# Performance work log

Measured on AMD Instinct MI355X. Metric: run time of the kernel, lower is better.

## Reference

```python
import jax, jax.numpy as jnp
import numpy as np

C = 1024        # BIGNET_DIM
GS = 128        # group_size
R = 4           # lora_dim
NL = 12         # 4 blocks x 3 QLoRALinear
N = 4096        # batch
NG = C * C // GS  # 8192 groups per layer
EPS = 1e-5


def dequant4(q4, norm):
    # q4: [NG, GS//2] int32 in [0,255] (two nibbles per byte), norm: [NG,1] f32
    low = q4 & 0xF
    high = (q4 >> 4) & 0xF
    # interleave: even positions = low nibble, odd = high nibble
    q8 = jnp.stack([low, high], axis=-1).reshape(q4.shape[0], GS)
    w = (q8.astype(jnp.float32) / 15.0 * 2.0 - 1.0) * norm
    return w.reshape(C, C)  # [out_features, in_features]


def qlora_linear(x, q4, norm, a, b):
    # base 4-bit dequant matmul + low-rank LoRA add (bias=False)
    w = dequant4(q4, norm)
    return x @ w.T + (x @ a.T) @ b.T  # [N,C]


def block(x, q4s, norms, As, Bs):
    h = qlora_linear(x, q4s[0], norms[0], As[0], Bs[0])
    h = jax.nn.relu(h)
    h = qlora_linear(h, q4s[1], norms[1], As[1], Bs[1])
    h = jax.nn.relu(h)
    h = qlora_linear(h, q4s[2], norms[2], As[2], Bs[2])
    return h + x  # residual


def layer_norm(x, g, b):
    mu = jnp.mean(x, axis=-1, keepdims=True)
    var = jnp.var(x, axis=-1, keepdims=True)
    return (x - mu) * jax.lax.rsqrt(var + EPS) * g + b


def setup_inputs() -> dict:
    key = jax.random.key(0)
    ks = jax.random.split(key, 5)
    x = jax.random.normal(ks[0], (N, C), dtype=jnp.float32)
    w_q4 = jax.random.randint(ks[1], (NL, NG, GS // 2), 0, 256, dtype=jnp.int32)
    w_norm = jax.random.uniform(ks[2], (NL, NG, 1), dtype=jnp.float32, minval=0.01, maxval=0.1)
    lora_a = jax.random.normal(ks[3], (NL, R, C), dtype=jnp.float32) * 0.02
    lora_b = jax.random.normal(ks[4], (NL, C, R), dtype=jnp.float32) * 0.02
    ln_g = jnp.ones((2, C), dtype=jnp.float32)
    ln_b = jnp.zeros((2, C), dtype=jnp.float32)
    return {"x": x, "w_q4": w_q4, "w_norm": w_norm, "lora_a": lora_a,
            "lora_b": lora_b, "ln_g": ln_g, "ln_b": ln_b}


def reference(x, w_q4, w_norm, lora_a, lora_b, ln_g, ln_b):
    h = block(x, w_q4[0:3], w_norm[0:3], lora_a[0:3], lora_b[0:3])
    h = layer_norm(h, ln_g[0], ln_b[0])
    h = block(h, w_q4[3:6], w_norm[3:6], lora_a[3:6], lora_b[3:6])
    h = block(h, w_q4[6:9], w_norm[6:9], lora_a[6:9], lora_b[6:9])
    h = layer_norm(h, ln_g[1], ln_b[1])
    h = block(h, w_q4[9:12], w_norm[9:12], lora_a[9:12], lora_b[9:12])
    return h
```

## Files before the change

### kernel.cpp

```cpp
#include <hip/hip_runtime.h>

#define CD 1024
#define NB 4096

typedef __attribute__((ext_vector_type(8))) short short8;
typedef __attribute__((ext_vector_type(4))) short short4v;
typedef __attribute__((ext_vector_type(4))) float f32x4;
typedef __attribute__((ext_vector_type(4))) int int4v;

typedef __attribute__((address_space(1))) const void gv_t;
typedef __attribute__((address_space(3))) void lv_t;
#define GLOAD16(g, l) __builtin_amdgcn_global_load_lds((gv_t*)(g), (lv_t*)(l), 16, 0, 0)

__device__ __forceinline__ short f2bf(float f) {
  unsigned u = __float_as_uint(f);
  u = (u + 0x7FFFu + ((u >> 16) & 1u)) >> 16;
  return (short)u;
}
__device__ __forceinline__ float bf2f(short s) {
  return __uint_as_float(((unsigned)(unsigned short)s) << 16);
}

__global__ __launch_bounds__(256) void prep_kernel(const float* __restrict__ x,
                                                   short* __restrict__ xb,
                                                   const int* __restrict__ q4,
                                                   const float* __restrict__ nrm,
                                                   const float* __restrict__ la,
                                                   const float* __restrict__ lb,
                                                   short* __restrict__ Wb) {
  int bid = blockIdx.x;
  if (bid < 2048) {
    int i = (bid * 256 + threadIdx.x) * 8;
    f32x4 a = *(const f32x4*)(x + i);
    f32x4 b = *(const f32x4*)(x + i + 4);
    short8 o;
    o[0] = f2bf(a[0]); o[1] = f2bf(a[1]); o[2] = f2bf(a[2]); o[3] = f2bf(a[3]);
    o[4] = f2bf(b[0]); o[5] = f2bf(b[1]); o[6] = f2bf(b[2]); o[7] = f2bf(b[3]);
    *(short8*)(xb + i) = o;
    return;
  }
  int tidg = (bid - 2048) * 256 + threadIdx.x;
  int w0 = tidg * 4;
  int l = w0 >> 19;
  int wl = w0 & 524287;
  int g = wl >> 6;
  int j0 = wl & 63;
  int o = g >> 3;
  int kb = ((g & 7) << 7) + (j0 << 1);
  int4v q = *(const int4v*)(q4 + w0);
  float n = nrm[(l << 13) + g];
  float s = n * (2.0f / 15.0f);
  f32x4 B = *(const f32x4*)(lb + (((l << 10) + o) << 2));
  const float* A = la + (l << 12);
  float Ar[4][8];
#pragma unroll
  for (int r = 0; r < 4; ++r) {
    f32x4 u = *(const f32x4*)(A + r * CD + kb);
    f32x4 v = *(const f32x4*)(A + r * CD + kb + 4);
    Ar[r][0] = u[0]; Ar[r][1] = u[1]; Ar[r][2] = u[2]; Ar[r][3] = u[3];
    Ar[r][4] = v[0]; Ar[r][5] = v[1]; Ar[r][6] = v[2]; Ar[r][7] = v[3];
  }
  short8 outv;
#pragma unroll
  for (int p = 0; p < 8; ++p) {
    int qw = q[p >> 1];
    int nib = (qw >> ((p & 1) << 2)) & 15;
    float wv = (float)nib * s - n;
    wv += B[0] * Ar[0][p] + B[1] * Ar[1][p] + B[2] * Ar[2][p] + B[3] * Ar[3][p];
    outv[p] = f2bf(wv);
  }
  *(short8*)(Wb + (l << 20) + (o << 10) + kb) = outv;
}

template <int EPI>
__global__ __launch_bounds__(512) void qgemm(const short* __restrict__ Act,
                                             const short* __restrict__ W,
                                             const short* __restrict__ Res,
                                             void* __restrict__ Out) {
  __shared__ __align__(16) short ldsA[2][2][128 * 64];
  __shared__ __align__(16) short ldsB[2][2][128 * 64];
  const int tid = threadIdx.x;
  const int lane = tid & 63;
  const int wid = tid >> 6;
  const int wr = wid >> 2;
  const int wc = wid & 3;
  const int f = blockIdx.x;
  const int xcd = f & 7, c = f >> 3;
  const int m0 = (((xcd << 2) | (c & 3)) << 7);
  const int o0 = ((c >> 2) << 7);

  const short* aptr[2][2];
  const short* bptr[2][2];
#pragma unroll
  for (int h = 0; h < 2; ++h)
#pragma unroll
    for (int i = 0; i < 2; ++i) {
      int cc = tid + (i << 9);
      int row = cc >> 3;
      int ch = (cc & 7) ^ (row & 7);
      aptr[h][i] = Act + (long)(m0 + row) * CD + (h << 6) + (ch << 3);
      bptr[h][i] = W + (long)(o0 + row) * CD + (h << 6) + (ch << 3);
    }

  auto stage = [&](int t, int buf) {
    const int koff = t << 7;
#pragma unroll
    for (int h = 0; h < 2; ++h)
#pragma unroll
      for (int i = 0; i < 2; ++i) {
        GLOAD16(aptr[h][i] + koff, &ldsA[buf][h][(tid + (i << 9)) << 3]);
        GLOAD16(bptr[h][i] + koff, &ldsB[buf][h][(tid + (i << 9)) << 3]);
      }
  };

  f32x4 acc[4][2] = {};
  const int frow = lane & 15;
  const int fch = lane >> 4;
  const int fsw = lane & 7;

  stage(0, 0);
  for (int t = 0; t < 8; ++t) {
    __syncthreads();
    if (t < 7) stage(t + 1, (t + 1) & 1);
#pragma unroll
    for (int kk = 0; kk < 4; ++kk) {
      const short* La = ldsA[t & 1][kk >> 1];
      const short* Lb = ldsB[t & 1][kk >> 1];
      const int chsw = (((kk & 1) << 2) + fch) ^ fsw;
      short8 af[4], wf[2];
#pragma unroll
      for (int m = 0; m < 4; ++m) {
        int row = (wr << 6) + (m << 4) + frow;
        af[m] = *(const short8*)(La + (row << 6) + (chsw << 3));
      }
#pragma unroll
      for (int n = 0; n < 2; ++n) {
        int row = (wc << 5) + (n << 4) + frow;
        wf[n] = *(const short8*)(Lb + (row << 6) + (chsw << 3));
      }
#pragma unroll
      for (int m = 0; m < 4; ++m)
#pragma unroll
        for (int n = 0; n < 2; ++n)
          acc[m][n] = __builtin_amdgcn_mfma_f32_16x16x32_bf16(wf[n], af[m], acc[m][n], 0, 0, 0);
    }
  }

  const int orow = m0 + (wr << 6) + frow;
  const int ocol = o0 + (wc << 5) + (fch << 2);
#pragma unroll
  for (int m = 0; m < 4; ++m) {
#pragma unroll
    for (int n = 0; n < 2; ++n) {
      long row = orow + (m << 4);
      int col = ocol + (n << 4);
      f32x4 v = acc[m][n];
      if (EPI == 0) {
        short4v ov;
        ov[0] = f2bf(fmaxf(v[0], 0.0f));
        ov[1] = f2bf(fmaxf(v[1], 0.0f));
        ov[2] = f2bf(fmaxf(v[2], 0.0f));
        ov[3] = f2bf(fmaxf(v[3], 0.0f));
        *(short4v*)((short*)Out + row * CD + col) = ov;
      } else if (EPI == 2) {
        short4v rv = *(const short4v*)(Res + row * CD + col);
        short4v ov;
        ov[0] = f2bf(v[0] + bf2f(rv[0]));
        ov[1] = f2bf(v[1] + bf2f(rv[1]));
        ov[2] = f2bf(v[2] + bf2f(rv[2]));
        ov[3] = f2bf(v[3] + bf2f(rv[3]));
        *(short4v*)((short*)Out + row * CD + col) = ov;
      } else {
        short4v rv = *(const short4v*)(Res + row * CD + col);
        f32x4 ov;
        ov[0] = v[0] + bf2f(rv[0]);
        ov[1] = v[1] + bf2f(rv[1]);
        ov[2] = v[2] + bf2f(rv[2]);
        ov[3] = v[3] + bf2f(rv[3]);
        *(f32x4*)((float*)Out + row * CD + col) = ov;
      }
    }
  }
}

__global__ __launch_bounds__(256) void ln_kernel(const short* __restrict__ in,
                                                 short* __restrict__ out,
                                                 const float* __restrict__ g,
                                                 const float* __restrict__ b) {
  __shared__ float rs_[4], rq_[4];
  int row = blockIdx.x, tid = threadIdx.x;
  int k = tid * 4;
  short4v v = *(const short4v*)(in + (long)row * CD + k);
  float f0 = bf2f(v[0]), f1 = bf2f(v[1]), f2 = bf2f(v[2]), f3 = bf2f(v[3]);
  float s = f0 + f1 + f2 + f3;
  float q = f0 * f0 + f1 * f1 + f2 * f2 + f3 * f3;
#pragma unroll
  for (int off = 1; off < 64; off <<= 1) {
    s += __shfl_xor(s, off);
    q += __shfl_xor(q, off);
  }
  if ((tid & 63) == 0) { rs_[tid >> 6] = s; rq_[tid >> 6] = q; }
  __syncthreads();
  s = rs_[0] + rs_[1] + rs_[2] + rs_[3];
  q = rq_[0] + rq_[1] + rq_[2] + rq_[3];
  float mu = s * (1.0f / 1024.0f);
  float var = q * (1.0f / 1024.0f) - mu * mu;
  float rstd = rsqrtf(var + 1e-5f);
  short4v o;
  o[0] = f2bf((f0 - mu) * rstd * g[k] + b[k]);
  o[1] = f2bf((f1 - mu) * rstd * g[k + 1] + b[k + 1]);
  o[2] = f2bf((f2 - mu) * rstd * g[k + 2] + b[k + 2]);
  o[3] = f2bf((f3 - mu) * rstd * g[k + 3] + b[k + 3]);
  *(short4v*)(out + (long)row * CD + k) = o;
}

extern "C" void kernel_launch(void* const* d_in, const int* in_sizes, int n_in,
                              void* d_out, int out_size, void* d_ws, size_t ws_size,
                              hipStream_t stream) {
  const float* x = (const float*)d_in[0];
  const int* q4 = (const int*)d_in[1];
  const float* nrm = (const float*)d_in[2];
  const float* la = (const float*)d_in[3];
  const float* lb = (const float*)d_in[4];
  const float* lng = (const float*)d_in[5];
  const float* lnb = (const float*)d_in[6];

  short* Wb = (short*)d_ws;
  short* buf0 = (short*)((char*)d_ws + (24u << 20));
  short* buf1 = buf0 + (long)NB * CD;
  short* buf2 = (short*)d_out;
  short* buf3 = buf2 + (long)NB * CD;
  float* outf = (float*)d_out;

  prep_kernel<<<dim3(8192), dim3(256), 0, stream>>>(x, buf0, q4, nrm, la, lb, Wb);

  dim3 gg(256), bb(512);
  auto Wl = [&](int l) { return Wb + ((long)l << 20); };

  qgemm<0><<<gg, bb, 0, stream>>>(buf0, Wl(0), nullptr, buf1);
  qgemm<0><<<gg, bb, 0, stream>>>(buf1, Wl(1), nullptr, buf2);
  qgemm<2><<<gg, bb, 0, stream>>>(buf2, Wl(2), buf0, buf3);
  ln_kernel<<<dim3(4096), dim3(256), 0, stream>>>(buf3, buf0, lng, lnb);
  qgemm<0><<<gg, bb, 0, stream>>>(buf0, Wl(3), nullptr, buf1);
  qgemm<0><<<gg, bb, 0, stream>>>(buf1, Wl(4), nullptr, buf2);
  qgemm<2><<<gg, bb, 0, stream>>>(buf2, Wl(5), buf0, buf3);
  qgemm<0><<<gg, bb, 0, stream>>>(buf3, Wl(6), nullptr, buf1);
  qgemm<0><<<gg, bb, 0, stream>>>(buf1, Wl(7), nullptr, buf2);
  qgemm<2><<<gg, bb, 0, stream>>>(buf2, Wl(8), buf3, buf0);
  ln_kernel<<<dim3(4096), dim3(256), 0, stream>>>(buf0, buf1, lng + CD, lnb + CD);
  qgemm<0><<<gg, bb, 0, stream>>>(buf1, Wl(9), nullptr, buf2);
  qgemm<0><<<gg, bb, 0, stream>>>(buf2, Wl(10), nullptr, buf0);
  qgemm<3><<<gg, bb, 0, stream>>>(buf0, Wl(11), buf1, (void*)outf);
}
```

Before: 278.9 us.

## Restructure qgemm main loop into triple-buffered 64-wide K pipeline with manual waitcnts

```diff
diff --git a/kernel.cpp b/kernel.cpp
--- a/kernel.cpp
+++ b/kernel.cpp
@@ -11,6 +11,7 @@
 typedef __attribute__((address_space(1))) const void gv_t;
 typedef __attribute__((address_space(3))) void lv_t;
 #define GLOAD16(g, l) __builtin_amdgcn_global_load_lds((gv_t*)(g), (lv_t*)(l), 16, 0, 0)
+#define MF(a, b, c) __builtin_amdgcn_mfma_f32_16x16x32_bf16((a), (b), (c), 0, 0, 0)
 
 __device__ __forceinline__ short f2bf(float f) {
   unsigned u = __float_as_uint(f);
@@ -77,8 +78,8 @@
                                              const short* __restrict__ W,
                                              const short* __restrict__ Res,
                                              void* __restrict__ Out) {
-  __shared__ __align__(16) short ldsA[2][2][128 * 64];
-  __shared__ __align__(16) short ldsB[2][2][128 * 64];
+  __shared__ __align__(16) short ldsA[3][128 * 64];
+  __shared__ __align__(16) short ldsB[3][128 * 64];
   const int tid = threadIdx.x;
   const int lane = tid & 63;
   const int wid = tid >> 6;
@@ -89,61 +90,87 @@
   const int m0 = (((xcd << 2) | (c & 3)) << 7);
   const int o0 = ((c >> 2) << 7);
 
-  const short* aptr[2][2];
-  const short* bptr[2][2];
-#pragma unroll
-  for (int h = 0; h < 2; ++h)
-#pragma unroll
-    for (int i = 0; i < 2; ++i) {
-      int cc = tid + (i << 9);
-      int row = cc >> 3;
-      int ch = (cc & 7) ^ (row & 7);
-      aptr[h][i] = Act + (long)(m0 + row) * CD + (h << 6) + (ch << 3);
-      bptr[h][i] = W + (long)(o0 + row) * CD + (h << 6) + (ch << 3);
-    }
-
-  auto stage = [&](int t, int buf) {
-    const int koff = t << 7;
-#pragma unroll
-    for (int h = 0; h < 2; ++h)
-#pragma unroll
-      for (int i = 0; i < 2; ++i) {
-        GLOAD16(aptr[h][i] + koff, &ldsA[buf][h][(tid + (i << 9)) << 3]);
-        GLOAD16(bptr[h][i] + koff, &ldsB[buf][h][(tid + (i << 9)) << 3]);
-      }
-  };
+  const short* asrc[2];
+  const short* bsrc[2];
+#pragma unroll
+  for (int i = 0; i < 2; ++i) {
+    int cc = tid + (i << 9);
+    int row = cc >> 3;
+    int ch = (cc & 7) ^ (row & 7);
+    asrc[i] = Act + (long)(m0 + row) * CD + (ch << 3);
+    bsrc[i] = W + (long)(o0 + row) * CD + (ch << 3);
+  }
 
   f32x4 acc[4][2] = {};
   const int frow = lane & 15;
   const int fch = lane >> 4;
   const int fsw = lane & 7;
 
-  stage(0, 0);
-  for (int t = 0; t < 8; ++t) {
-    __syncthreads();
-    if (t < 7) stage(t + 1, (t + 1) & 1);
-#pragma unroll
-    for (int kk = 0; kk < 4; ++kk) {
-      const short* La = ldsA[t & 1][kk >> 1];
-      const short* Lb = ldsB[t & 1][kk >> 1];
-      const int chsw = (((kk & 1) << 2) + fch) ^ fsw;
-      short8 af[4], wf[2];
-#pragma unroll
-      for (int m = 0; m < 4; ++m) {
-        int row = (wr << 6) + (m << 4) + frow;
-        af[m] = *(const short8*)(La + (row << 6) + (chsw << 3));
+#pragma unroll
+  for (int pt = 0; pt < 2; ++pt) {
+    const int koff = pt << 6;
+    GLOAD16(asrc[0] + koff, &ldsA[pt][(tid) << 3]);
+    GLOAD16(asrc[1] + koff, &ldsA[pt][(tid + 512) << 3]);
+    GLOAD16(bsrc[0] + koff, &ldsB[pt][(tid) << 3]);
+    GLOAD16(bsrc[1] + koff, &ldsB[pt][(tid + 512) << 3]);
+  }
+
+  int t3 = 0;
+  for (int t = 0; t < 16; ++t) {
+    const short* La = ldsA[t3];
+    const short* Lb = ldsB[t3];
+    const int b2 = (t3 == 0) ? 2 : t3 - 1;
+    const int koff2 = (t + 2) << 6;
+    if (t < 15) asm volatile("s_waitcnt vmcnt(4)" ::: "memory");
+    else        asm volatile("s_waitcnt vmcnt(0)" ::: "memory");
+    __builtin_amdgcn_sched_barrier(0);
+    __builtin_amdgcn_s_barrier();
+    __builtin_amdgcn_sched_barrier(0);
+    {
+      const int chsw = fch ^ fsw;
+      short8 af0 = *(const short8*)(La + (((wr << 6) + 0  + frow) << 6) + (chsw << 3));
+      short8 af1 = *(const short8*)(La + (((wr << 6) + 16 + frow) << 6) + (chsw << 3));
+      short8 af2 = *(const short8*)(La + (((wr << 6) + 32 + frow) << 6) + (chsw << 3));
+      short8 af3 = *(const short8*)(La + (((wr << 6) + 48 + frow) << 6) + (chsw << 3));
+      short8 wf0 = *(const short8*)(Lb + (((wc << 5) + 0  + frow) << 6) + (chsw << 3));
+      short8 wf1 = *(const short8*)(Lb + (((wc << 5) + 16 + frow) << 6) + (chsw << 3));
+      if (t < 14) {
+        GLOAD16(asrc[0] + koff2, &ldsA[b2][(tid) << 3]);
+        GLOAD16(asrc[1] + koff2, &ldsA[b2][(tid + 512) << 3]);
       }
-#pragma unroll
-      for (int n = 0; n < 2; ++n) {
-        int row = (wc << 5) + (n << 4) + frow;
-        wf[n] = *(const short8*)(Lb + (row << 6) + (chsw << 3));
+      asm volatile("s_waitcnt lgkmcnt(0)" ::: "memory");
+      __builtin_amdgcn_sched_barrier(0);
+      __builtin_amdgcn_s_setprio(1);
+      acc[0][0] = MF(wf0, af0, acc[0][0]); acc[0][1] = MF(wf1, af0, acc[0][1]);
+      acc[1][0] = MF(wf0, af1, acc[1][0]); acc[1][1] = MF(wf1, af1, acc[1][1]);
+      acc[2][0] = MF(wf0, af2, acc[2][0]); acc[2][1] = MF(wf1, af2, acc[2][1]);
+      acc[3][0] = MF(wf0, af3, acc[3][0]); acc[3][1] = MF(wf1, af3, acc[3][1]);
+      __builtin_amdgcn_s_setprio(0);
+    }
+    __builtin_amdgcn_s_barrier();
+    __builtin_amdgcn_sched_barrier(0);
+    {
+      const int chsw = (4 + fch) ^ fsw;
+      short8 af0 = *(const short8*)(La + (((wr << 6) + 0  + frow) << 6) + (chsw << 3));
+      short8 af1 = *(const short8*)(La + (((wr << 6) + 16 + frow) << 6) + (chsw << 3));
+      short8 af2 = *(const short8*)(La + (((wr << 6) + 32 + frow) << 6) + (chsw << 3));
+      short8 af3 = *(const short8*)(La + (((wr << 6) + 48 + frow) << 6) + (chsw << 3));
+      short8 wf0 = *(const short8*)(Lb + (((wc << 5) + 0  + frow) << 6) + (chsw << 3));
+      short8 wf1 = *(const short8*)(Lb + (((wc << 5) + 16 + frow) << 6) + (chsw << 3));
+      if (t < 14) {
+        GLOAD16(bsrc[0] + koff2, &ldsB[b2][(tid) << 3]);
+        GLOAD16(bsrc[1] + koff2, &ldsB[b2][(tid + 512) << 3]);
       }
-#pragma unroll
-      for (int m = 0; m < 4; ++m)
-#pragma unroll
-        for (int n = 0; n < 2; ++n)
-          acc[m][n] = __builtin_amdgcn_mfma_f32_16x16x32_bf16(wf[n], af[m], acc[m][n], 0, 0, 0);
+      asm volatile("s_waitcnt lgkmcnt(0)" ::: "memory");
+      __builtin_amdgcn_sched_barrier(0);
+      __builtin_amdgcn_s_setprio(1);
+      acc[0][0] = MF(wf0, af0, acc[0][0]); acc[0][1] = MF(wf1, af0, acc[0][1]);
+      acc[1][0] = MF(wf0, af1, acc[1][0]); acc[1][1] = MF(wf1, af1, acc[1][1]);
+      acc[2][0] = MF(wf0, af2, acc[2][0]); acc[2][1] = MF(wf1, af2, acc[2][1]);
+      acc[3][0] = MF(wf0, af3, acc[3][0]); acc[3][1] = MF(wf1, af3, acc[3][1]);
+      __builtin_amdgcn_s_setprio(0);
     }
+    t3 = (t3 == 2) ? 0 : t3 + 1;
   }
 
   const int orow = m0 + (wr << 6) + frow;
```

Measured after the change: 297.7 us. 1.07x slower.

## Fuse all layers into one cooperative persistent kernel with grid syncs

Applied to the files above, without the earlier changes.

```diff
diff --git a/kernel.cpp b/kernel.cpp
--- a/kernel.cpp
+++ b/kernel.cpp
@@ -1,4 +1,7 @@
 #include <hip/hip_runtime.h>
+#include <hip/hip_cooperative_groups.h>
+
+namespace cg = cooperative_groups;
 
 #define CD 1024
 #define NB 4096
@@ -11,6 +14,7 @@
 typedef __attribute__((address_space(1))) const void gv_t;
 typedef __attribute__((address_space(3))) void lv_t;
 #define GLOAD16(g, l) __builtin_amdgcn_global_load_lds((gv_t*)(g), (lv_t*)(l), 16, 0, 0)
+#define MF(a, b, c) __builtin_amdgcn_mfma_f32_16x16x32_bf16((a), (b), (c), 0, 0, 0)
 
 __device__ __forceinline__ short f2bf(float f) {
   unsigned u = __float_as_uint(f);
@@ -21,64 +25,11 @@
   return __uint_as_float(((unsigned)(unsigned short)s) << 16);
 }
 
-__global__ __launch_bounds__(256) void prep_kernel(const float* __restrict__ x,
-                                                   short* __restrict__ xb,
-                                                   const int* __restrict__ q4,
-                                                   const float* __restrict__ nrm,
-                                                   const float* __restrict__ la,
-                                                   const float* __restrict__ lb,
-                                                   short* __restrict__ Wb) {
-  int bid = blockIdx.x;
-  if (bid < 2048) {
-    int i = (bid * 256 + threadIdx.x) * 8;
-    f32x4 a = *(const f32x4*)(x + i);
-    f32x4 b = *(const f32x4*)(x + i + 4);
-    short8 o;
-    o[0] = f2bf(a[0]); o[1] = f2bf(a[1]); o[2] = f2bf(a[2]); o[3] = f2bf(a[3]);
-    o[4] = f2bf(b[0]); o[5] = f2bf(b[1]); o[6] = f2bf(b[2]); o[7] = f2bf(b[3]);
-    *(short8*)(xb + i) = o;
-    return;
-  }
-  int tidg = (bid - 2048) * 256 + threadIdx.x;
-  int w0 = tidg * 4;
-  int l = w0 >> 19;
-  int wl = w0 & 524287;
-  int g = wl >> 6;
-  int j0 = wl & 63;
-  int o = g >> 3;
-  int kb = ((g & 7) << 7) + (j0 << 1);
-  int4v q = *(const int4v*)(q4 + w0);
-  float n = nrm[(l << 13) + g];
-  float s = n * (2.0f / 15.0f);
-  f32x4 B = *(const f32x4*)(lb + (((l << 10) + o) << 2));
-  const float* A = la + (l << 12);
-  float Ar[4][8];
-#pragma unroll
-  for (int r = 0; r < 4; ++r) {
-    f32x4 u = *(const f32x4*)(A + r * CD + kb);
-    f32x4 v = *(const f32x4*)(A + r * CD + kb + 4);
-    Ar[r][0] = u[0]; Ar[r][1] = u[1]; Ar[r][2] = u[2]; Ar[r][3] = u[3];
-    Ar[r][4] = v[0]; Ar[r][5] = v[1]; Ar[r][6] = v[2]; Ar[r][7] = v[3];
-  }
-  short8 outv;
-#pragma unroll
-  for (int p = 0; p < 8; ++p) {
-    int qw = q[p >> 1];
-    int nib = (qw >> ((p & 1) << 2)) & 15;
-    float wv = (float)nib * s - n;
-    wv += B[0] * Ar[0][p] + B[1] * Ar[1][p] + B[2] * Ar[2][p] + B[3] * Ar[3][p];
-    outv[p] = f2bf(wv);
-  }
-  *(short8*)(Wb + (l << 20) + (o << 10) + kb) = outv;
-}
-
-template <int EPI>
-__global__ __launch_bounds__(512) void qgemm(const short* __restrict__ Act,
-                                             const short* __restrict__ W,
-                                             const short* __restrict__ Res,
-                                             void* __restrict__ Out) {
-  __shared__ __align__(16) short ldsA[2][2][128 * 64];
-  __shared__ __align__(16) short ldsB[2][2][128 * 64];
+__device__ __noinline__ void gemm_layer(const short* __restrict__ Act,
+                                        const short* __restrict__ W,
+                                        const short* __restrict__ Res,
+                                        void* __restrict__ Out, int epi,
+                                        short* ldsA, short* ldsB) {
   const int tid = threadIdx.x;
   const int lane = tid & 63;
   const int wid = tid >> 6;
@@ -108,8 +59,8 @@
     for (int h = 0; h < 2; ++h)
 #pragma unroll
       for (int i = 0; i < 2; ++i) {
-        GLOAD16(aptr[h][i] + koff, &ldsA[buf][h][(tid + (i << 9)) << 3]);
-        GLOAD16(bptr[h][i] + koff, &ldsB[buf][h][(tid + (i << 9)) << 3]);
+        GLOAD16(aptr[h][i] + koff, ldsA + ((buf << 1) + h) * 8192 + ((tid + (i << 9)) << 3));
+        GLOAD16(bptr[h][i] + koff, ldsB + ((buf << 1) + h) * 8192 + ((tid + (i << 9)) << 3));
       }
   };
 
@@ -124,8 +75,8 @@
     if (t < 7) stage(t + 1, (t + 1) & 1);
 #pragma unroll
     for (int kk = 0; kk < 4; ++kk) {
-      const short* La = ldsA[t & 1][kk >> 1];
-      const short* Lb = ldsB[t & 1][kk >> 1];
+      const short* La = ldsA + (((t & 1) << 1) + (kk >> 1)) * 8192;
+      const short* Lb = ldsB + (((t & 1) << 1) + (kk >> 1)) * 8192;
       const int chsw = (((kk & 1) << 2) + fch) ^ fsw;
       short8 af[4], wf[2];
 #pragma unroll
@@ -142,9 +93,10 @@
       for (int m = 0; m < 4; ++m)
 #pragma unroll
         for (int n = 0; n < 2; ++n)
-          acc[m][n] = __builtin_amdgcn_mfma_f32_16x16x32_bf16(wf[n], af[m], acc[m][n], 0, 0, 0);
-    }
-  }
+          acc[m][n] = MF(wf[n], af[m], acc[m][n]);
+    }
+  }
+  __syncthreads();
 
   const int orow = m0 + (wr << 6) + frow;
   const int ocol = o0 + (wc << 5) + (fch << 2);
@@ -155,14 +107,14 @@
       long row = orow + (m << 4);
       int col = ocol + (n << 4);
       f32x4 v = acc[m][n];
-      if (EPI == 0) {
+      if (epi == 0) {
         short4v ov;
         ov[0] = f2bf(fmaxf(v[0], 0.0f));
         ov[1] = f2bf(fmaxf(v[1], 0.0f));
         ov[2] = f2bf(fmaxf(v[2], 0.0f));
         ov[3] = f2bf(fmaxf(v[3], 0.0f));
         *(short4v*)((short*)Out + row * CD + col) = ov;
-      } else if (EPI == 2) {
+      } else if (epi == 2) {
         short4v rv = *(const short4v*)(Res + row * CD + col);
         short4v ov;
         ov[0] = f2bf(v[0] + bf2f(rv[0]));
@@ -183,35 +135,120 @@
   }
 }
 
-__global__ __launch_bounds__(256) void ln_kernel(const short* __restrict__ in,
-                                                 short* __restrict__ out,
-                                                 const float* __restrict__ g,
-                                                 const float* __restrict__ b) {
-  __shared__ float rs_[4], rq_[4];
-  int row = blockIdx.x, tid = threadIdx.x;
-  int k = tid * 4;
-  short4v v = *(const short4v*)(in + (long)row * CD + k);
-  float f0 = bf2f(v[0]), f1 = bf2f(v[1]), f2 = bf2f(v[2]), f3 = bf2f(v[3]);
-  float s = f0 + f1 + f2 + f3;
-  float q = f0 * f0 + f1 * f1 + f2 * f2 + f3 * f3;
-#pragma unroll
-  for (int off = 1; off < 64; off <<= 1) {
-    s += __shfl_xor(s, off);
-    q += __shfl_xor(q, off);
-  }
-  if ((tid & 63) == 0) { rs_[tid >> 6] = s; rq_[tid >> 6] = q; }
-  __syncthreads();
-  s = rs_[0] + rs_[1] + rs_[2] + rs_[3];
-  q = rq_[0] + rq_[1] + rq_[2] + rq_[3];
-  float mu = s * (1.0f / 1024.0f);
-  float var = q * (1.0f / 1024.0f) - mu * mu;
-  float rstd = rsqrtf(var + 1e-5f);
-  short4v o;
-  o[0] = f2bf((f0 - mu) * rstd * g[k] + b[k]);
-  o[1] = f2bf((f1 - mu) * rstd * g[k + 1] + b[k + 1]);
-  o[2] = f2bf((f2 - mu) * rstd * g[k + 2] + b[k + 2]);
-  o[3] = f2bf((f3 - mu) * rstd * g[k + 3] + b[k + 3]);
-  *(short4v*)(out + (long)row * CD + k) = o;
+__device__ __noinline__ void ln_16rows(const short* __restrict__ in,
+                                       short* __restrict__ out,
+                                       const float* __restrict__ g,
+                                       const float* __restrict__ b,
+                                       float* red) {
+  const int tid = threadIdx.x;
+  const int half = tid >> 8;
+  const int tin = tid & 255;
+  const int wid = tid >> 6;
+  const int k = tin << 2;
+  for (int it = 0; it < 8; ++it) {
+    long row = (blockIdx.x << 4) + (it << 1) + half;
+    short4v v = *(const short4v*)(in + (row << 10) + k);
+    float f0 = bf2f(v[0]), f1 = bf2f(v[1]), f2 = bf2f(v[2]), f3 = bf2f(v[3]);
+    float s = f0 + f1 + f2 + f3;
+    float q = f0 * f0 + f1 * f1 + f2 * f2 + f3 * f3;
+#pragma unroll
+    for (int off = 1; off < 64; off <<= 1) {
+      s += __shfl_xor(s, off);
+      q += __shfl_xor(q, off);
+    }
+    if ((tid & 63) == 0) { red[wid] = s; red[8 + wid] = q; }
+    __syncthreads();
+    int base = half << 2;
+    s = red[base] + red[base + 1] + red[base + 2] + red[base + 3];
+    q = red[8 + base] + red[9 + base] + red[10 + base] + red[11 + base];
+    float mu = s * (1.0f / 1024.0f);
+    float var = q * (1.0f / 1024.0f) - mu * mu;
+    float rstd = rsqrtf(var + 1e-5f);
+    short4v o;
+    o[0] = f2bf((f0 - mu) * rstd * g[k] + b[k]);
+    o[1] = f2bf((f1 - mu) * rstd * g[k + 1] + b[k + 1]);
+    o[2] = f2bf((f2 - mu) * rstd * g[k + 2] + b[k + 2]);
+    o[3] = f2bf((f3 - mu) * rstd * g[k + 3] + b[k + 3]);
+    *(short4v*)(out + (row << 10) + k) = o;
+    __syncthreads();
+  }
+}
+
+__global__ __launch_bounds__(512, 1) void mega(const float* __restrict__ x,
+                                               const int* __restrict__ q4,
+                                               const float* __restrict__ nrm,
+                                               const float* __restrict__ la,
+                                               const float* __restrict__ lb,
+                                               const float* __restrict__ lng,
+                                               const float* __restrict__ lnb,
+                                               short* Wb, short* buf0, short* buf1,
+                                               short* buf2, short* buf3, float* outf) {
+  cg::grid_group grid = cg::this_grid();
+  __shared__ __align__(16) short ldsA[2 * 2 * 8192];
+  __shared__ __align__(16) short ldsB[2 * 2 * 8192];
+  __shared__ float red[16];
+  const int gtid = blockIdx.x * 512 + threadIdx.x;
+
+  for (int cc = gtid; cc < 524288; cc += 131072) {
+    int i = cc << 3;
+    f32x4 a = *(const f32x4*)(x + i);
+    f32x4 b = *(const f32x4*)(x + i + 4);
+    short8 o;
+    o[0] = f2bf(a[0]); o[1] = f2bf(a[1]); o[2] = f2bf(a[2]); o[3] = f2bf(a[3]);
+    o[4] = f2bf(b[0]); o[5] = f2bf(b[1]); o[6] = f2bf(b[2]); o[7] = f2bf(b[3]);
+    *(short8*)(buf0 + i) = o;
+  }
+  for (int tg = gtid; tg < 1572864; tg += 131072) {
+    int w0 = tg * 4;
+    int l = w0 >> 19;
+    int wl = w0 & 524287;
+    int g = wl >> 6;
+    int j0 = wl & 63;
+    int o = g >> 3;
+    int kb = ((g & 7) << 7) + (j0 << 1);
+    int4v q = *(const int4v*)(q4 + w0);
+    float n = nrm[(l << 13) + g];
+    float s = n * (2.0f / 15.0f);
+    f32x4 B = *(const f32x4*)(lb + (((l << 10) + o) << 2));
+    const float* A = la + (l << 12);
+    float Ar[4][8];
+#pragma unroll
+    for (int r = 0; r < 4; ++r) {
+      f32x4 u = *(const f32x4*)(A + r * CD + kb);
+      f32x4 v = *(const f32x4*)(A + r * CD + kb + 4);
+      Ar[r][0] = u[0]; Ar[r][1] = u[1]; Ar[r][2] = u[2]; Ar[r][3] = u[3];
+      Ar[r][4] = v[0]; Ar[r][5] = v[1]; Ar[r][6] = v[2]; Ar[r][7] = v[3];
+    }
+    short8 outv;
+#pragma unroll
+    for (int p = 0; p < 8; ++p) {
+      int qw = q[p >> 1];
+      int nib = (qw >> ((p & 1) << 2)) & 15;
+      float wv = (float)nib * s - n;
+      wv += B[0] * Ar[0][p] + B[1] * Ar[1][p] + B[2] * Ar[2][p] + B[3] * Ar[3][p];
+      outv[p] = f2bf(wv);
+    }
+    *(short8*)(Wb + (l << 20) + (o << 10) + kb) = outv;
+  }
+  grid.sync();
+
+  short* W0 = Wb;
+#define WL(l) (W0 + ((long)(l) << 20))
+  gemm_layer(buf0, WL(0), nullptr, buf1, 0, ldsA, ldsB); grid.sync();
+  gemm_layer(buf1, WL(1), nullptr, buf2, 0, ldsA, ldsB); grid.sync();
+  gemm_layer(buf2, WL(2), buf0, buf3, 2, ldsA, ldsB);    grid.sync();
+  ln_16rows(buf3, buf0, lng, lnb, red);                  grid.sync();
+  gemm_layer(buf0, WL(3), nullptr, buf1, 0, ldsA, ldsB); grid.sync();
+  gemm_layer(buf1, WL(4), nullptr, buf2, 0, ldsA, ldsB); grid.sync();
+  gemm_layer(buf2, WL(5), buf0, buf3, 2, ldsA, ldsB);    grid.sync();
+  gemm_layer(buf3, WL(6), nullptr, buf1, 0, ldsA, ldsB); grid.sync();
+  gemm_layer(buf1, WL(7), nullptr, buf2, 0, ldsA, ldsB); grid.sync();
+  gemm_layer(buf2, WL(8), buf3, buf0, 2, ldsA, ldsB);    grid.sync();
+  ln_16rows(buf0, buf1, lng + CD, lnb + CD, red);        grid.sync();
+  gemm_layer(buf1, WL(9), nullptr, buf2, 0, ldsA, ldsB); grid.sync();
+  gemm_layer(buf2, WL(10), nullptr, buf0, 0, ldsA, ldsB); grid.sync();
+  gemm_layer(buf0, WL(11), buf1, outf, 3, ldsA, ldsB);
+#undef WL
 }
 
 extern "C" void kernel_launch(void* const* d_in, const int* in_sizes, int n_in,
@@ -232,23 +269,7 @@
   short* buf3 = buf2 + (long)NB * CD;
   float* outf = (float*)d_out;
 
-  prep_kernel<<<dim3(8192), dim3(256), 0, stream>>>(x, buf0, q4, nrm, la, lb, Wb);
-
-  dim3 gg(256), bb(512);
-  auto Wl = [&](int l) { return Wb + ((long)l << 20); };
-
-  qgemm<0><<<gg, bb, 0, stream>>>(buf0, Wl(0), nullptr, buf1);
-  qgemm<0><<<gg, bb, 0, stream>>>(buf1, Wl(1), nullptr, buf2);
-  qgemm<2><<<gg, bb, 0, stream>>>(buf2, Wl(2), buf0, buf3);
-  ln_kernel<<<dim3(4096), dim3(256), 0, stream>>>(buf3, buf0, lng, lnb);
-  qgemm<0><<<gg, bb, 0, stream>>>(buf0, Wl(3), nullptr, buf1);
-  qgemm<0><<<gg, bb, 0, stream>>>(buf1, Wl(4), nullptr, buf2);
-  qgemm<2><<<gg, bb, 0, stream>>>(buf2, Wl(5), buf0, buf3);
-  qgemm<0><<<gg, bb, 0, stream>>>(buf3, Wl(6), nullptr, buf1);
-  qgemm<0><<<gg, bb, 0, stream>>>(buf1, Wl(7), nullptr, buf2);
-  qgemm<2><<<gg, bb, 0, stream>>>(buf2, Wl(8), buf3, buf0);
-  ln_kernel<<<dim3(4096), dim3(256), 0, stream>>>(buf0, buf1, lng + CD, lnb + CD);
-  qgemm<0><<<gg, bb, 0, stream>>>(buf1, Wl(9), nullptr, buf2);
-  qgemm<0><<<gg, bb, 0, stream>>>(buf2, Wl(10), nullptr, buf0);
-  qgemm<3><<<gg, bb, 0, stream>>>(buf0, Wl(11), buf1, (void*)outf);
-}
+  void* args[] = {&x, &q4, &nrm, &la, &lb, &lng, &lnb,
+                  &Wb, &buf0, &buf1, &buf2, &buf3, &outf};
+  hipLaunchCooperativeKernel((void*)mega, dim3(256), dim3(512), args, 0, stream);
+}
```

Result: slower. 612.5 us (+119.6%).
